# Kernel optimization log

Hardware: AMD Instinct MI355X
Metric: run time of the kernel (lower is better)

Reference implementation:

```python
import jax, jax.numpy as jnp
import numpy as np

RES = 28      # input feature-map resolution
RES2 = 14     # ceil(RES/2) after downsample
NH = 8        # num_heads
KD = 16       # key_dim
D = 64        # attn_ratio * key_dim (per-head value dim)
DH = 512      # D * NH
N = RES * RES
N2 = RES2 * RES2


def _rel_idx():
    # Matches tf.meshgrid default 'xy' indexing in set_attention_bias_idxs.
    r = RES
    kp = np.stack(np.meshgrid(np.arange(r), np.arange(r), indexing='xy')).reshape(2, -1)
    qp = np.stack(np.meshgrid(np.arange(0, r, 2), np.arange(0, r, 2), indexing='xy')).reshape(2, -1)
    rel = np.abs(qp[:, :, None] - kp[:, None, :])
    return jnp.asarray(rel[0] * r + rel[1], dtype=jnp.int32)  # [N2, N]

REL_IDX = _rel_idx()


def _dw_stride2(x, w, b):
    # Depthwise 3x3 conv, stride 2, TF 'SAME' padding. w: [3,3,1,C]
    c = x.shape[-1]
    y = jax.lax.conv_general_dilated(
        x, w, window_strides=(2, 2), padding='SAME',
        dimension_numbers=('NHWC', 'HWIO', 'NHWC'), feature_group_count=c)
    return y + b


def setup_inputs() -> dict:
    key = jax.random.key(0)
    ks = jax.random.split(key, 10)
    f = jnp.float32
    C, OUT = 384, 768
    return {
        'x': jax.random.normal(ks[0], (64, RES, RES, C), f),
        'q_local_w': jax.random.normal(ks[1], (3, 3, 1, C), f) * 0.1,
        'q_local_b': jnp.zeros((C,), f),
        'q_proj_w': jax.random.normal(ks[2], (C, NH * KD), f) * 0.05,
        'q_proj_b': jnp.zeros((NH * KD,), f),
        'q_bn_s': jnp.ones((NH * KD,), f),
        'q_bn_b': jnp.zeros((NH * KD,), f),
        'k_w': jax.random.normal(ks[3], (C, NH * KD), f) * 0.05,
        'k_b': jnp.zeros((NH * KD,), f),
        'k_bn_s': jnp.ones((NH * KD,), f),
        'k_bn_b': jnp.zeros((NH * KD,), f),
        'v_w': jax.random.normal(ks[4], (C, DH), f) * 0.05,
        'v_b': jnp.zeros((DH,), f),
        'v_bn_s': jnp.ones((DH,), f),
        'v_bn_b': jnp.zeros((DH,), f),
        'vloc_w': jax.random.normal(ks[5], (3, 3, 1, DH), f) * 0.1,
        'vloc_b': jnp.zeros((DH,), f),
        'vloc_bn_s': jnp.ones((DH,), f),
        'vloc_bn_b': jnp.zeros((DH,), f),
        'proj_w': jax.random.normal(ks[6], (DH, OUT), f) * 0.05,
        'proj_b': jnp.zeros((OUT,), f),
        'proj_bn_s': jnp.ones((OUT,), f),
        'proj_bn_b': jnp.zeros((OUT,), f),
        'attn_bias': jax.random.normal(ks[7], (NH, N), f) * 0.1,
    }


def reference(x, q_local_w, q_local_b, q_proj_w, q_proj_b, q_bn_s, q_bn_b,
              k_w, k_b, k_bn_s, k_bn_b, v_w, v_b, v_bn_s, v_bn_b,
              vloc_w, vloc_b, vloc_bn_s, vloc_bn_b,
              proj_w, proj_b, proj_bn_s, proj_bn_b, attn_bias):
    B = x.shape[0]
    scale = KD ** -0.5
    # LGQuery: depthwise-conv local branch + 1x1 avg-pool (stride-2 subsample)
    q = _dw_stride2(x, q_local_w, q_local_b) + x[:, ::2, ::2, :]
    q = (q @ q_proj_w + q_proj_b) * q_bn_s + q_bn_b          # [B,14,14,128]
    k = (x @ k_w + k_b) * k_bn_s + k_bn_b                    # [B,28,28,128]
    v = (x @ v_w + v_b) * v_bn_s + v_bn_b                    # [B,28,28,512]
    v_local = _dw_stride2(v, vloc_w, vloc_b) * vloc_bn_s + vloc_bn_b  # [B,14,14,512]
    qh = q.reshape(B, N2, NH, KD).transpose(0, 2, 1, 3)      # [B,H,N2,KD]
    kh = k.reshape(B, N, NH, KD).transpose(0, 2, 3, 1)       # [B,H,KD,N]
    vh = v.reshape(B, N, NH, D).transpose(0, 2, 1, 3)        # [B,H,N,D]
    attn = (qh @ kh) * scale + attn_bias[:, REL_IDX]         # [B,H,N2,N]
    attn = jax.nn.softmax(attn, axis=-1)
    out = (attn @ vh).transpose(0, 2, 1, 3).reshape(B, RES2, RES2, DH)
    out = out + v_local
    # proj: Activation(None) is identity -> 1x1 conv + BN(inference)
    return (out @ proj_w + proj_b) * proj_bn_s + proj_bn_b   # [B,14,14,768]
```

## Files before the change

### kernel.cpp

```cpp
#include <hip/hip_runtime.h>
#include <cstdint>

#define RES    28
#define RES2   14
#define NHEAD  8
#define KDIM   16
#define DV     64
#define DHID   512
#define NSEQ   784
#define N2SEQ  196
#define BATCH  64
#define CIN    384

typedef unsigned short u16;
typedef short  short4_t __attribute__((ext_vector_type(4)));
typedef short  short8_t __attribute__((ext_vector_type(8)));
typedef float  f32x4  __attribute__((ext_vector_type(4)));
typedef u16    us4    __attribute__((ext_vector_type(4)));
typedef u16    us8    __attribute__((ext_vector_type(8)));

__device__ __forceinline__ u16 f2bf(float f) {
    uint32_t u = __float_as_uint(f);
    return (u16)((u + 0x7fffu + ((u >> 16) & 1u)) >> 16);
}
__device__ __forceinline__ float bf2f(u16 h) {
    return __uint_as_float(((uint32_t)h) << 16);
}

__global__ __launch_bounds__(256)
void cast_bf16_kernel(const float* __restrict__ in, u16* __restrict__ out, int n4)
{
    int i = blockIdx.x * 256 + threadIdx.x;
    if (i >= n4) return;
    float4 v = ((const float4*)in)[i];
    us4 r;
    r.x = f2bf(v.x); r.y = f2bf(v.y); r.z = f2bf(v.z); r.w = f2bf(v.w);
    ((us4*)out)[i] = r;
}

__global__ __launch_bounds__(256)
void castT_kernel(const float* __restrict__ W, u16* __restrict__ Wt, int K, int N)
{
    int i = blockIdx.x * 256 + threadIdx.x;
    if (i >= K * N) return;
    int n = i / K, k = i % K;
    Wt[i] = f2bf(W[(size_t)k * N + n]);
}

#define TM 128
#define TN 128
#define TK 32

template<int OUT_BF16>
__global__ __launch_bounds__(256)
void gemm_mfma_kernel(const u16* __restrict__ A, const u16* __restrict__ Bt,
                      const float* __restrict__ bias, const float* __restrict__ scale,
                      const float* __restrict__ shift, void* __restrict__ outp,
                      int M, int N, int K)
{
    __shared__ u16 As[TM * TK];
    __shared__ u16 Bs[TN * TK];

    const int t  = threadIdx.x;
    const int w  = t >> 6;
    const int li = t & 63;
    const int wm = w >> 1, wn = w & 1;
    const int bm = blockIdx.x * TM;
    const int bn = blockIdx.y * TN;
    const int m16 = li & 15;
    const int kg  = li >> 4;

    f32x4 acc[4][4];
    #pragma unroll
    for (int i = 0; i < 4; ++i)
        #pragma unroll
        for (int j = 0; j < 4; ++j) acc[i][j] = (f32x4)0.0f;

    for (int k0 = 0; k0 < K; k0 += TK) {
        #pragma unroll
        for (int i = 0; i < 2; ++i) {
            int c   = (w * 2 + i) * 64 + li;
            int row = c >> 2, kc = c & 3;
            const u16* ag = A  + (size_t)(bm + row) * K + k0 + kc * 8;
            const u16* bg = Bt + (size_t)(bn + row) * K + k0 + kc * 8;
            char* la = (char*)As + (size_t)(w * 2 + i) * 64 * 16;
            char* lb = (char*)Bs + (size_t)(w * 2 + i) * 64 * 16;
            __builtin_amdgcn_global_load_lds(
                (const __attribute__((address_space(1))) void*)ag,
                (__attribute__((address_space(3))) void*)la, 16, 0, 0);
            __builtin_amdgcn_global_load_lds(
                (const __attribute__((address_space(1))) void*)bg,
                (__attribute__((address_space(3))) void*)lb, 16, 0, 0);
        }
        __syncthreads();

        short8_t af[4], bf[4];
        #pragma unroll
        for (int mi = 0; mi < 4; ++mi)
            af[mi] = *(const short8_t*)&As[(wm * 64 + mi * 16 + m16) * TK + kg * 8];
        #pragma unroll
        for (int ni = 0; ni < 4; ++ni)
            bf[ni] = *(const short8_t*)&Bs[(wn * 64 + ni * 16 + m16) * TK + kg * 8];

        #pragma unroll
        for (int mi = 0; mi < 4; ++mi)
            #pragma unroll
            for (int ni = 0; ni < 4; ++ni)
                acc[mi][ni] = __builtin_amdgcn_mfma_f32_16x16x32_bf16(
                    af[mi], bf[ni], acc[mi][ni], 0, 0, 0);
        __syncthreads();
    }

    #pragma unroll
    for (int ni = 0; ni < 4; ++ni) {
        const int col = bn + wn * 64 + ni * 16 + m16;
        const float bi = bias[col], sc = scale[col], sh = shift[col];
        #pragma unroll
        for (int mi = 0; mi < 4; ++mi) {
            const int rbase = bm + wm * 64 + mi * 16 + kg * 4;
            #pragma unroll
            for (int r = 0; r < 4; ++r) {
                float val = (acc[mi][ni][r] + bi) * sc + sh;
                if (OUT_BF16)
                    ((u16*)outp)[(size_t)(rbase + r) * N + col] = f2bf(val);
                else
                    ((float*)outp)[(size_t)(rbase + r) * N + col] = val;
            }
        }
    }
}

__global__ __launch_bounds__(256)
void qin_kernel(const float* __restrict__ x, const float* __restrict__ w,
                const float* __restrict__ b, u16* __restrict__ qin)
{
    const int C4 = CIN / 4;
    int idx = blockIdx.x * 256 + threadIdx.x;
    if (idx >= BATCH * RES2 * RES2 * C4) return;
    int c4 = idx % C4;
    int r  = idx / C4;
    int j  = r % RES2; r /= RES2;
    int i  = r % RES2;
    int bb = r / RES2;

    const float4* x4 = (const float4*)x;
    const float4* w4 = (const float4*)w;
    float4 acc = make_float4(0.f, 0.f, 0.f, 0.f);
    #pragma unroll
    for (int dy = 0; dy < 3; ++dy) {
        int iy = 2 * i + dy;
        if (iy >= RES) continue;
        #pragma unroll
        for (int dx = 0; dx < 3; ++dx) {
            int ix = 2 * j + dx;
            if (ix >= RES) continue;
            float4 xv = x4[((size_t)(bb * RES + iy) * RES + ix) * C4 + c4];
            float4 wv = w4[(dy * 3 + dx) * C4 + c4];
            acc.x += xv.x * wv.x; acc.y += xv.y * wv.y;
            acc.z += xv.z * wv.z; acc.w += xv.w * wv.w;
        }
    }
    float4 bv = ((const float4*)b)[c4];
    float4 xs = x4[((size_t)(bb * RES + 2 * i) * RES + 2 * j) * C4 + c4];
    us4 o;
    o.x = f2bf(acc.x + bv.x + xs.x);
    o.y = f2bf(acc.y + bv.y + xs.y);
    o.z = f2bf(acc.z + bv.z + xs.z);
    o.w = f2bf(acc.w + bv.w + xs.w);
    ((us4*)qin)[idx] = o;
}

__global__ __launch_bounds__(256)
void vloc_kernel(const u16* __restrict__ v, const float* __restrict__ w,
                 const float* __restrict__ b, const float* __restrict__ s,
                 const float* __restrict__ sh, u16* __restrict__ out)
{
    const int C4 = DHID / 4;
    int idx = blockIdx.x * 256 + threadIdx.x;
    if (idx >= BATCH * RES2 * RES2 * C4) return;
    int c4 = idx % C4;
    int r  = idx / C4;
    int j  = r % RES2; r /= RES2;
    int i  = r % RES2;
    int bb = r / RES2;

    const us4* v4 = (const us4*)v;
    const float4* w4 = (const float4*)w;
    float4 acc = make_float4(0.f, 0.f, 0.f, 0.f);
    #pragma unroll
    for (int dy = 0; dy < 3; ++dy) {
        int iy = 2 * i + dy;
        if (iy >= RES) continue;
        #pragma unroll
        for (int dx = 0; dx < 3; ++dx) {
            int ix = 2 * j + dx;
            if (ix >= RES) continue;
            us4 xu = v4[((size_t)(bb * RES + iy) * RES + ix) * C4 + c4];
            float4 wv = w4[(dy * 3 + dx) * C4 + c4];
            acc.x += bf2f(xu.x) * wv.x; acc.y += bf2f(xu.y) * wv.y;
            acc.z += bf2f(xu.z) * wv.z; acc.w += bf2f(xu.w) * wv.w;
        }
    }
    float4 bv = ((const float4*)b)[c4];
    float4 sv = ((const float4*)s)[c4];
    float4 hv = ((const float4*)sh)[c4];
    us4 o;
    o.x = f2bf((acc.x + bv.x) * sv.x + hv.x);
    o.y = f2bf((acc.y + bv.y) * sv.y + hv.y);
    o.z = f2bf((acc.z + bv.z) * sv.z + hv.z);
    o.w = f2bf((acc.w + bv.w) * sv.w + hv.w);
    ((us4*)out)[idx] = o;
}

__global__ __launch_bounds__(256)
void vt_transpose_kernel(const u16* __restrict__ vbuf, u16* __restrict__ vt)
{
    __shared__ u16 tile[64][66];
    const int t  = threadIdx.x;
    const int b  = blockIdx.x;
    const int k0 = blockIdx.y * 64;
    const int h  = blockIdx.z;

    {
        int kr = t >> 2, cc = (t & 3) * 16;
        int key = k0 + kr;
        if (key < NSEQ) {
            const u16* src = vbuf + ((size_t)b * NSEQ + key) * DHID + h * 64 + cc;
            us8 v0 = *(const us8*)src;
            us8 v1 = *(const us8*)(src + 8);
            #pragma unroll
            for (int i = 0; i < 8; ++i) { tile[kr][cc + i] = v0[i]; tile[kr][cc + 8 + i] = v1[i]; }
        }
    }
    __syncthreads();
    {
        int cr = t >> 2, kc = (t & 3) * 16;
        if (k0 + kc < NSEQ) {
            us8 o0, o1;
            #pragma unroll
            for (int i = 0; i < 8; ++i) { o0[i] = tile[kc + i][cr]; o1[i] = tile[kc + 8 + i][cr]; }
            u16* dst = vt + (((size_t)b * NHEAD + h) * 64 + cr) * NSEQ + k0 + kc;
            *(us8*)dst = o0;
            *(us8*)(dst + 8) = o1;
        }
    }
}

__global__ __launch_bounds__(256)
void biasT_kernel(const float* __restrict__ bias, float* __restrict__ biasT)
{
    int tid = blockIdx.x * 256 + threadIdx.x;
    if (tid >= NHEAD * NSEQ * N2SEQ) return;
    int q   = tid % N2SEQ;
    int rem = tid / N2SEQ;
    int key = rem % NSEQ;
    int h   = rem / NSEQ;
    int pi = q / 14, pj = q % 14;
    int ku = key / 28, kw = key % 28;
    int d0 = 2 * pj - kw; if (d0 < 0) d0 = -d0;
    int d1 = 2 * pi - ku; if (d1 < 0) d1 = -d1;
    biasT[tid] = bias[h * NSEQ + d0 * 28 + d1];
}

__global__ __launch_bounds__(128)
void attn_mfma_kernel(const u16* __restrict__ q, const u16* __restrict__ k,
                      const u16* __restrict__ vt, const float* __restrict__ biasT,
                      u16* __restrict__ io)
{
    __shared__ u16 Ks[64 * 16];
    __shared__ u16 Vs[64 * 68];

    const int t    = threadIdx.x;
    const int w    = t >> 6;
    const int lane = t & 63;
    const int col  = lane & 15;
    const int quad = lane >> 4;
    const int bh = blockIdx.x;
    const int b  = bh >> 3;
    const int h  = bh & 7;
    const int qtile = blockIdx.y * 2 + w;
    const bool qvalid = qtile * 16 < N2SEQ;
    const int qbase = qvalid ? qtile * 16 : 192;

    int qq = qbase + col; if (qq > 195) qq = 195;
    short8_t qf = (short8_t)0;
    if (quad < 2)
        qf = *(const short8_t*)(q + ((size_t)(b * N2SEQ + qq) * 128) + h * 16 + quad * 8);

    f32x4 O[4];
    #pragma unroll
    for (int i = 0; i < 4; ++i) O[i] = (f32x4)0.0f;
    float m = -3e38f, l = 0.f;

    const u16* vtb = vt + (size_t)bh * 64 * NSEQ;

    for (int ti = 0; ti < 13; ++ti) {
        const int t0 = ti * 64;
        {
            int c = w * 64 + lane;
            int row = c >> 1;
            int tok = t0 + row; if (tok > 783) tok = 783;
            const u16* src = k + ((size_t)(b * NSEQ + tok) * 128) + h * 16 + (c & 1) * 8;
            char* dst = (char*)Ks + w * 1024;
            __builtin_amdgcn_global_load_lds(
                (const __attribute__((address_space(1))) void*)src,
                (__attribute__((address_space(3))) void*)dst, 16, 0, 0);
        }
        {
            int d = t >> 1, pr = t & 1;
            const u16* src = vtb + (size_t)d * NSEQ;
            u16* dst = Vs + d * 68 + pr * 32;
            #pragma unroll
            for (int i = 0; i < 4; ++i) {
                int kk = t0 + pr * 32 + i * 8; if (kk > 776) kk = 776;
                us8 vv = *(const us8*)(src + kk);
                us4 lo, hi;
                lo.x = vv[0]; lo.y = vv[1]; lo.z = vv[2]; lo.w = vv[3];
                hi.x = vv[4]; hi.y = vv[5]; hi.z = vv[6]; hi.w = vv[7];
                *(us4*)(dst + i * 8)     = lo;
                *(us4*)(dst + i * 8 + 4) = hi;
            }
        }
        __syncthreads();

        f32x4 S[4];
        #pragma unroll
        for (int ks = 0; ks < 4; ++ks) {
            short8_t kf = (short8_t)0;
            if (quad < 2)
                kf = *(const short8_t*)&Ks[(ks * 16 + col) * 16 + quad * 8];
            S[ks] = __builtin_amdgcn_mfma_f32_16x16x32_bf16(kf, qf, (f32x4)0.0f, 0, 0, 0);
        }

        float p[16];
        float mt = -3e38f;
        #pragma unroll
        for (int ks = 0; ks < 4; ++ks) {
            #pragma unroll
            for (int r = 0; r < 4; ++r) {
                int key = t0 + ks * 16 + quad * 4 + r;
                float lg;
                if (key < NSEQ)
                    lg = S[ks][r] * 0.25f + biasT[((size_t)h * NSEQ + key) * N2SEQ + qbase + col];
                else
                    lg = -1e30f;
                p[ks * 4 + r] = lg;
                mt = fmaxf(mt, lg);
            }
        }
        mt = fmaxf(mt, __shfl_xor(mt, 16));
        mt = fmaxf(mt, __shfl_xor(mt, 32));
        float mnew = fmaxf(m, mt);
        float alpha = __expf(m - mnew);
        m = mnew;
        float s = 0.f;
        #pragma unroll
        for (int i = 0; i < 16; ++i) { p[i] = __expf(p[i] - mnew); s += p[i]; }
        s += __shfl_xor(s, 16);
        s += __shfl_xor(s, 32);
        l = l * alpha + s;

        float ar[4];
        #pragma unroll
        for (int r = 0; r < 4; ++r) ar[r] = __shfl(alpha, quad * 4 + r);
        #pragma unroll
        for (int ns = 0; ns < 4; ++ns)
            #pragma unroll
            for (int r = 0; r < 4; ++r) O[ns][r] *= ar[r];

        short8_t pf[2];
        #pragma unroll
        for (int pr = 0; pr < 2; ++pr)
            #pragma unroll
            for (int j = 0; j < 8; ++j)
                pf[pr][j] = (short)f2bf(p[(2 * pr + (j >> 2)) * 4 + (j & 3)]);

        #pragma unroll
        for (int ns = 0; ns < 4; ++ns) {
            #pragma unroll
            for (int pr = 0; pr < 2; ++pr) {
                const u16* vrow = &Vs[(ns * 16 + col) * 68 + pr * 32 + quad * 4];
                us4 v0 = *(const us4*)vrow;
                us4 v1 = *(const us4*)(vrow + 16);
                short8_t vf;
                vf[0] = (short)v0.x; vf[1] = (short)v0.y; vf[2] = (short)v0.z; vf[3] = (short)v0.w;
                vf[4] = (short)v1.x; vf[5] = (short)v1.y; vf[6] = (short)v1.z; vf[7] = (short)v1.w;
                O[ns] = __builtin_amdgcn_mfma_f32_16x16x32_bf16(pf[pr], vf, O[ns], 0, 0, 0);
            }
        }
        __syncthreads();
    }

    float linv = 1.0f / l;
    float lr[4];
    #pragma unroll
    for (int r = 0; r < 4; ++r) lr[r] = __shfl(linv, quad * 4 + r);

    if (qvalid) {
        #pragma unroll
        for (int ns = 0; ns < 4; ++ns) {
            #pragma unroll
            for (int r = 0; r < 4; ++r) {
                int qg2 = qbase + quad * 4 + r;
                if (qg2 < N2SEQ) {
                    size_t a = ((size_t)(b * N2SEQ + qg2) * DHID) + h * 64 + ns * 16 + col;
                    io[a] = f2bf(O[ns][r] * lr[r] + bf2f(io[a]));
                }
            }
        }
    }
}

extern "C" void kernel_launch(void* const* d_in, const int* in_sizes, int n_in,
                              void* d_out, int out_size, void* d_ws, size_t ws_size,
                              hipStream_t stream)
{
    const float* x          = (const float*)d_in[0];
    const float* q_local_w  = (const float*)d_in[1];
    const float* q_local_b  = (const float*)d_in[2];
    const float* q_proj_w   = (const float*)d_in[3];
    const float* q_proj_b   = (const float*)d_in[4];
    const float* q_bn_s     = (const float*)d_in[5];
    const float* q_bn_b     = (const float*)d_in[6];
    const float* k_w        = (const float*)d_in[7];
    const float* k_b        = (const float*)d_in[8];
    const float* k_bn_s     = (const float*)d_in[9];
    const float* k_bn_b     = (const float*)d_in[10];
    const float* v_w        = (const float*)d_in[11];
    const float* v_b        = (const float*)d_in[12];
    const float* v_bn_s     = (const float*)d_in[13];
    const float* v_bn_b     = (const float*)d_in[14];
    const float* vloc_w     = (const float*)d_in[15];
    const float* vloc_b     = (const float*)d_in[16];
    const float* vloc_bn_s  = (const float*)d_in[17];
    const float* vloc_bn_b  = (const float*)d_in[18];
    const float* proj_w     = (const float*)d_in[19];
    const float* proj_b     = (const float*)d_in[20];
    const float* proj_bn_s  = (const float*)d_in[21];
    const float* proj_bn_b  = (const float*)d_in[22];
    const float* attn_bias  = (const float*)d_in[23];
    float* out = (float*)d_out;

    const int M1 = BATCH * NSEQ;
    const int M2 = BATCH * N2SEQ;

    char* p = (char*)d_ws;
    u16* xb     = (u16*)p;
    u16* qin_bf = (u16*)(p + 38535168);
    u16* vt     = (u16*)p;
    size_t off = 51380224;
    u16* kwt = (u16*)(p + off);
    u16* vwt = kwt + (size_t)CIN * 128;
    u16* qwt = vwt + (size_t)CIN * DHID;
    u16* pwt = qwt + (size_t)CIN * 128;
    off += 1376256;
    u16* kbuf = (u16*)(p + off);    off += (size_t)M1 * 128 * 2;
    u16* vbuf = (u16*)(p + off);    off += (size_t)M1 * DHID * 2;
    u16* qbuf = (u16*)(p + off);    off += (size_t)M2 * 128 * 2;
    u16* vloc_bf = (u16*)(p + off); off += (size_t)M2 * DHID * 2;
    float* biasT = (float*)(p + off);

    {
        int n4 = M1 * CIN / 4;
        cast_bf16_kernel<<<dim3((n4 + 255) / 256), 256, 0, stream>>>(x, xb, n4);
    }
    castT_kernel<<<dim3((CIN * 128 + 255) / 256), 256, 0, stream>>>(k_w, kwt, CIN, 128);
    castT_kernel<<<dim3((CIN * DHID + 255) / 256), 256, 0, stream>>>(v_w, vwt, CIN, DHID);
    castT_kernel<<<dim3((CIN * 128 + 255) / 256), 256, 0, stream>>>(q_proj_w, qwt, CIN, 128);
    castT_kernel<<<dim3((DHID * 768 + 255) / 256), 256, 0, stream>>>(proj_w, pwt, DHID, 768);
    biasT_kernel<<<dim3((NHEAD * NSEQ * N2SEQ + 255) / 256), 256, 0, stream>>>(attn_bias, biasT);

    {
        int items = M2 * (CIN / 4);
        qin_kernel<<<dim3((items + 255) / 256), 256, 0, stream>>>(x, q_local_w, q_local_b, qin_bf);
    }
    gemm_mfma_kernel<1><<<dim3(M1 / TM, 128 / TN), 256, 0, stream>>>(
        xb, kwt, k_b, k_bn_s, k_bn_b, kbuf, M1, 128, CIN);
    gemm_mfma_kernel<1><<<dim3(M1 / TM, DHID / TN), 256, 0, stream>>>(
        xb, vwt, v_b, v_bn_s, v_bn_b, vbuf, M1, DHID, CIN);
    gemm_mfma_kernel<1><<<dim3(M2 / TM, 128 / TN), 256, 0, stream>>>(
        qin_bf, qwt, q_proj_b, q_bn_s, q_bn_b, qbuf, M2, 128, CIN);

    vt_transpose_kernel<<<dim3(BATCH, 13, NHEAD), 256, 0, stream>>>(vbuf, vt);

    {
        int items = M2 * (DHID / 4);
        vloc_kernel<<<dim3((items + 255) / 256), 256, 0, stream>>>(
            vbuf, vloc_w, vloc_b, vloc_bn_s, vloc_bn_b, vloc_bf);
    }
    attn_mfma_kernel<<<dim3(BATCH * NHEAD, 7), 128, 0, stream>>>(
        qbuf, kbuf, vt, biasT, vloc_bf);

    gemm_mfma_kernel<0><<<dim3(M2 / TM, 768 / TN), 256, 0, stream>>>(
        vloc_bf, pwt, proj_b, proj_bn_s, proj_bn_b, out, M2, 768, DHID);
}
```

Measured before the change: 450.9 us.

## Restructure attention: one block per batch-head, MFMA-layout bias, head-major Q/K

Each attention block now handles all 13 query tiles of a batch-head with 4 waves, so K/V tiles load into LDS once per batch-head instead of once per pair of query tiles. The relative-position bias is precomputed in MFMA accumulator layout and fed as the MFMA C input, with masking folded in. The 0.25 softmax scale is folded into the Q projection's BN scale and shift. Q and K GEMMs write head-major layout for contiguous loads. In exchange, each thread holds more registers (4 sets of O/m/l), and the grid shrinks to 512 blocks, which may lower occupancy.

```diff
diff --git a/kernel.cpp b/kernel.cpp
--- a/kernel.cpp
+++ b/kernel.cpp
@@ -13,7 +13,6 @@
 #define CIN    384
 
 typedef unsigned short u16;
-typedef short  short4_t __attribute__((ext_vector_type(4)));
 typedef short  short8_t __attribute__((ext_vector_type(8)));
 typedef float  f32x4  __attribute__((ext_vector_type(4)));
 typedef u16    us4    __attribute__((ext_vector_type(4)));
@@ -47,16 +46,57 @@
     Wt[i] = f2bf(W[(size_t)k * N + n]);
 }
 
+__global__ void scale_qsb_kernel(const float* __restrict__ s, const float* __restrict__ b,
+                                 float* __restrict__ o)
+{
+    int i = threadIdx.x;
+    o[i] = 0.25f * s[i];
+    o[128 + i] = 0.25f * b[i];
+}
+
+__global__ __launch_bounds__(256)
+void biasC_kernel(const float* __restrict__ bias, float* __restrict__ biasC)
+{
+    int tid = blockIdx.x * 256 + threadIdx.x;
+    if (tid >= NHEAD * 13 * 4 * 13 * 64) return;
+    int lane = tid & 63;
+    int rem  = tid >> 6;
+    int qt = rem % 13; rem /= 13;
+    int ks = rem % 4;  rem /= 4;
+    int ti = rem % 13;
+    int h  = rem / 13;
+    int col = lane & 15, quad = lane >> 4;
+    int q = qt * 16 + col;
+    float4 out;
+    float* po = &out.x;
+    #pragma unroll
+    for (int r = 0; r < 4; ++r) {
+        int key = ti * 64 + ks * 16 + quad * 4 + r;
+        float v;
+        if (key >= NSEQ || q >= N2SEQ) {
+            v = -1e30f;
+        } else {
+            int pi = q / 14, pj = q % 14;
+            int ku = key / 28, kw = key % 28;
+            int d0 = 2 * pj - kw; if (d0 < 0) d0 = -d0;
+            int d1 = 2 * pi - ku; if (d1 < 0) d1 = -d1;
+            v = bias[h * NSEQ + d0 * 28 + d1];
+        }
+        po[r] = v;
+    }
+    ((float4*)biasC)[tid] = out;
+}
+
 #define TM 128
 #define TN 128
 #define TK 32
 
-template<int OUT_BF16>
+template<int OUT_MODE>
 __global__ __launch_bounds__(256)
 void gemm_mfma_kernel(const u16* __restrict__ A, const u16* __restrict__ Bt,
                       const float* __restrict__ bias, const float* __restrict__ scale,
                       const float* __restrict__ shift, void* __restrict__ outp,
-                      int M, int N, int K)
+                      int M, int N, int K, int rpb)
 {
     __shared__ u16 As[TM * TK];
     __shared__ u16 Bs[TN * TK];
@@ -121,10 +161,16 @@
             #pragma unroll
             for (int r = 0; r < 4; ++r) {
                 float val = (acc[mi][ni][r] + bi) * sc + sh;
-                if (OUT_BF16)
-                    ((u16*)outp)[(size_t)(rbase + r) * N + col] = f2bf(val);
-                else
-                    ((float*)outp)[(size_t)(rbase + r) * N + col] = val;
+                const int row = rbase + r;
+                if (OUT_MODE == 0) {
+                    ((float*)outp)[(size_t)row * N + col] = val;
+                } else if (OUT_MODE == 1) {
+                    ((u16*)outp)[(size_t)row * N + col] = f2bf(val);
+                } else {
+                    int bb = row / rpb, tok = row % rpb;
+                    int hh = col >> 4;
+                    ((u16*)outp)[((size_t)(bb * NHEAD + hh) * rpb + tok) * 16 + (col & 15)] = f2bf(val);
+                }
             }
         }
     }
@@ -246,25 +292,9 @@
     }
 }
 
-__global__ __launch_bounds__(256)
-void biasT_kernel(const float* __restrict__ bias, float* __restrict__ biasT)
-{
-    int tid = blockIdx.x * 256 + threadIdx.x;
-    if (tid >= NHEAD * NSEQ * N2SEQ) return;
-    int q   = tid % N2SEQ;
-    int rem = tid / N2SEQ;
-    int key = rem % NSEQ;
-    int h   = rem / NSEQ;
-    int pi = q / 14, pj = q % 14;
-    int ku = key / 28, kw = key % 28;
-    int d0 = 2 * pj - kw; if (d0 < 0) d0 = -d0;
-    int d1 = 2 * pi - ku; if (d1 < 0) d1 = -d1;
-    biasT[tid] = bias[h * NSEQ + d0 * 28 + d1];
-}
-
-__global__ __launch_bounds__(128)
+__global__ __launch_bounds__(256, 2)
 void attn_mfma_kernel(const u16* __restrict__ q, const u16* __restrict__ k,
-                      const u16* __restrict__ vt, const float* __restrict__ biasT,
+                      const u16* __restrict__ vt, const float* __restrict__ biasC,
                       u16* __restrict__ io)
 {
     __shared__ u16 Ks[64 * 16];
@@ -275,138 +305,163 @@
     const int lane = t & 63;
     const int col  = lane & 15;
     const int quad = lane >> 4;
-    const int bh = blockIdx.x;
-    const int b  = bh >> 3;
-    const int h  = bh & 7;
-    const int qtile = blockIdx.y * 2 + w;
-    const bool qvalid = qtile * 16 < N2SEQ;
-    const int qbase = qvalid ? qtile * 16 : 192;
-
-    int qq = qbase + col; if (qq > 195) qq = 195;
-    short8_t qf = (short8_t)0;
-    if (quad < 2)
-        qf = *(const short8_t*)(q + ((size_t)(b * N2SEQ + qq) * 128) + h * 16 + quad * 8);
-
-    f32x4 O[4];
-    #pragma unroll
-    for (int i = 0; i < 4; ++i) O[i] = (f32x4)0.0f;
-    float m = -3e38f, l = 0.f;
+    const int h  = blockIdx.x >> 6;
+    const int b  = blockIdx.x & 63;
+    const int bh = b * NHEAD + h;
+
+    short8_t qf[4];
+    #pragma unroll
+    for (int i = 0; i < 4; ++i) {
+        int qt = w + 4 * i;
+        qf[i] = (short8_t)0;
+        if (qt < 13 && quad < 2) {
+            int qq = qt * 16 + col; if (qq > 195) qq = 195;
+            qf[i] = *(const short8_t*)(q + ((size_t)bh * N2SEQ + qq) * 16 + quad * 8);
+        }
+    }
+
+    f32x4 O[4][4];
+    float m[4], l[4];
+    #pragma unroll
+    for (int i = 0; i < 4; ++i) {
+        m[i] = -3e38f; l[i] = 0.f;
+        #pragma unroll
+        for (int ns = 0; ns < 4; ++ns) O[i][ns] = (f32x4)0.0f;
+    }
 
     const u16* vtb = vt + (size_t)bh * 64 * NSEQ;
+    const u16* kb  = k + (size_t)bh * NSEQ * 16;
 
     for (int ti = 0; ti < 13; ++ti) {
         const int t0 = ti * 64;
-        {
+        if (w < 2) {
             int c = w * 64 + lane;
-            int row = c >> 1;
-            int tok = t0 + row; if (tok > 783) tok = 783;
-            const u16* src = k + ((size_t)(b * NSEQ + tok) * 128) + h * 16 + (c & 1) * 8;
+            int tok = t0 + (c >> 1); if (tok > 783) tok = 783;
+            const u16* src = kb + (size_t)tok * 16 + (c & 1) * 8;
             char* dst = (char*)Ks + w * 1024;
             __builtin_amdgcn_global_load_lds(
                 (const __attribute__((address_space(1))) void*)src,
                 (__attribute__((address_space(3))) void*)dst, 16, 0, 0);
         }
         {
-            int d = t >> 1, pr = t & 1;
+            int d = t >> 2, part = t & 3;
             const u16* src = vtb + (size_t)d * NSEQ;
-            u16* dst = Vs + d * 68 + pr * 32;
-            #pragma unroll
-            for (int i = 0; i < 4; ++i) {
-                int kk = t0 + pr * 32 + i * 8; if (kk > 776) kk = 776;
-                us8 vv = *(const us8*)(src + kk);
-                us4 lo, hi;
-                lo.x = vv[0]; lo.y = vv[1]; lo.z = vv[2]; lo.w = vv[3];
-                hi.x = vv[4]; hi.y = vv[5]; hi.z = vv[6]; hi.w = vv[7];
-                *(us4*)(dst + i * 8)     = lo;
-                *(us4*)(dst + i * 8 + 4) = hi;
-            }
+            u16* dst = Vs + d * 68 + part * 16;
+            int kk = t0 + part * 16;
+            int k0a = kk     > 776 ? 776 : kk;
+            int k1a = kk + 8 > 776 ? 776 : kk + 8;
+            us8 v0 = *(const us8*)(src + k0a);
+            us8 v1 = *(const us8*)(src + k1a);
+            us4 a, bb2, c2, d2;
+            a.x = v0[0]; a.y = v0[1]; a.z = v0[2]; a.w = v0[3];
+            bb2.x = v0[4]; bb2.y = v0[5]; bb2.z = v0[6]; bb2.w = v0[7];
+            c2.x = v1[0]; c2.y = v1[1]; c2.z = v1[2]; c2.w = v1[3];
+            d2.x = v1[4]; d2.y = v1[5]; d2.z = v1[6]; d2.w = v1[7];
+            *(us4*)(dst)      = a;
+            *(us4*)(dst + 4)  = bb2;
+            *(us4*)(dst + 8)  = c2;
+            *(us4*)(dst + 12) = d2;
         }
         __syncthreads();
 
-        f32x4 S[4];
+        short8_t kf[4];
         #pragma unroll
         for (int ks = 0; ks < 4; ++ks) {
-            short8_t kf = (short8_t)0;
+            kf[ks] = (short8_t)0;
             if (quad < 2)
-                kf = *(const short8_t*)&Ks[(ks * 16 + col) * 16 + quad * 8];
-            S[ks] = __builtin_amdgcn_mfma_f32_16x16x32_bf16(kf, qf, (f32x4)0.0f, 0, 0, 0);
-        }
-
-        float p[16];
-        float mt = -3e38f;
-        #pragma unroll
-        for (int ks = 0; ks < 4; ++ks) {
-            #pragma unroll
-            for (int r = 0; r < 4; ++r) {
-                int key = t0 + ks * 16 + quad * 4 + r;
-                float lg;
-                if (key < NSEQ)
-                    lg = S[ks][r] * 0.25f + biasT[((size_t)h * NSEQ + key) * N2SEQ + qbase + col];
-                else
-                    lg = -1e30f;
-                p[ks * 4 + r] = lg;
-                mt = fmaxf(mt, lg);
-            }
-        }
-        mt = fmaxf(mt, __shfl_xor(mt, 16));
-        mt = fmaxf(mt, __shfl_xor(mt, 32));
-        float mnew = fmaxf(m, mt);
-        float alpha = __expf(m - mnew);
-        m = mnew;
-        float s = 0.f;
-        #pragma unroll
-        for (int i = 0; i < 16; ++i) { p[i] = __expf(p[i] - mnew); s += p[i]; }
-        s += __shfl_xor(s, 16);
-        s += __shfl_xor(s, 32);
-        l = l * alpha + s;
-
-        float ar[4];
-        #pragma unroll
-        for (int r = 0; r < 4; ++r) ar[r] = __shfl(alpha, quad * 4 + r);
+                kf[ks] = *(const short8_t*)&Ks[(ks * 16 + col) * 16 + quad * 8];
+        }
+        short8_t vf[4][2];
         #pragma unroll
         for (int ns = 0; ns < 4; ++ns)
-            #pragma unroll
-            for (int r = 0; r < 4; ++r) O[ns][r] *= ar[r];
-
-        short8_t pf[2];
-        #pragma unroll
-        for (int pr = 0; pr < 2; ++pr)
-            #pragma unroll
-            for (int j = 0; j < 8; ++j)
-                pf[pr][j] = (short)f2bf(p[(2 * pr + (j >> 2)) * 4 + (j & 3)]);
-
-        #pragma unroll
-        for (int ns = 0; ns < 4; ++ns) {
             #pragma unroll
             for (int pr = 0; pr < 2; ++pr) {
                 const u16* vrow = &Vs[(ns * 16 + col) * 68 + pr * 32 + quad * 4];
                 us4 v0 = *(const us4*)vrow;
                 us4 v1 = *(const us4*)(vrow + 16);
-                short8_t vf;
-                vf[0] = (short)v0.x; vf[1] = (short)v0.y; vf[2] = (short)v0.z; vf[3] = (short)v0.w;
-                vf[4] = (short)v1.x; vf[5] = (short)v1.y; vf[6] = (short)v1.z; vf[7] = (short)v1.w;
-                O[ns] = __builtin_amdgcn_mfma_f32_16x16x32_bf16(pf[pr], vf, O[ns], 0, 0, 0);
+                short8_t vv;
+                vv[0] = (short)v0.x; vv[1] = (short)v0.y; vv[2] = (short)v0.z; vv[3] = (short)v0.w;
+                vv[4] = (short)v1.x; vv[5] = (short)v1.y; vv[6] = (short)v1.z; vv[7] = (short)v1.w;
+                vf[ns][pr] = vv;
             }
+
+        #pragma unroll
+        for (int i = 0; i < 4; ++i) {
+            int qt = w + 4 * i;
+            if (qt < 13) {
+                f32x4 S[4];
+                #pragma unroll
+                for (int ks = 0; ks < 4; ++ks) {
+                    f32x4 c = *(const f32x4*)(biasC +
+                        ((((size_t)h * 13 + ti) * 4 + ks) * 13 + qt) * 256 + lane * 4);
+                    S[ks] = __builtin_amdgcn_mfma_f32_16x16x32_bf16(kf[ks], qf[i], c, 0, 0, 0);
+                }
+                float p[16];
+                float mt = -3e38f;
+                #pragma unroll
+                for (int ks = 0; ks < 4; ++ks)
+                    #pragma unroll
+                    for (int r = 0; r < 4; ++r) {
+                        float lg = S[ks][r];
+                        p[ks * 4 + r] = lg;
+                        mt = fmaxf(mt, lg);
+                    }
+                mt = fmaxf(mt, __shfl_xor(mt, 16));
+                mt = fmaxf(mt, __shfl_xor(mt, 32));
+                float mnew = fmaxf(m[i], mt);
+                float alpha = __expf(m[i] - mnew);
+                m[i] = mnew;
+                float s = 0.f;
+                #pragma unroll
+                for (int j = 0; j < 16; ++j) { p[j] = __expf(p[j] - mnew); s += p[j]; }
+                s += __shfl_xor(s, 16);
+                s += __shfl_xor(s, 32);
+                l[i] = l[i] * alpha + s;
+
+                float ar[4];
+                #pragma unroll
+                for (int r = 0; r < 4; ++r) ar[r] = __shfl(alpha, quad * 4 + r);
+                #pragma unroll
+                for (int ns = 0; ns < 4; ++ns)
+                    #pragma unroll
+                    for (int r = 0; r < 4; ++r) O[i][ns][r] *= ar[r];
+
+                short8_t pf[2];
+                #pragma unroll
+                for (int pr = 0; pr < 2; ++pr)
+                    #pragma unroll
+                    for (int j = 0; j < 8; ++j)
+                        pf[pr][j] = (short)f2bf(p[(2 * pr + (j >> 2)) * 4 + (j & 3)]);
+
+                #pragma unroll
+                for (int ns = 0; ns < 4; ++ns)
+                    #pragma unroll
+                    for (int pr = 0; pr < 2; ++pr)
+                        O[i][ns] = __builtin_amdgcn_mfma_f32_16x16x32_bf16(
+                            pf[pr], vf[ns][pr], O[i][ns], 0, 0, 0);
+            }
         }
         __syncthreads();
     }
 
-    float linv = 1.0f / l;
-    float lr[4];
-    #pragma unroll
-    for (int r = 0; r < 4; ++r) lr[r] = __shfl(linv, quad * 4 + r);
-
-    if (qvalid) {
-        #pragma unroll
-        for (int ns = 0; ns < 4; ++ns) {
-            #pragma unroll
-            for (int r = 0; r < 4; ++r) {
-                int qg2 = qbase + quad * 4 + r;
-                if (qg2 < N2SEQ) {
-                    size_t a = ((size_t)(b * N2SEQ + qg2) * DHID) + h * 64 + ns * 16 + col;
-                    io[a] = f2bf(O[ns][r] * lr[r] + bf2f(io[a]));
+    #pragma unroll
+    for (int i = 0; i < 4; ++i) {
+        int qt = w + 4 * i;
+        if (qt < 13) {
+            float linv = 1.0f / l[i];
+            float lr[4];
+            #pragma unroll
+            for (int r = 0; r < 4; ++r) lr[r] = __shfl(linv, quad * 4 + r);
+            #pragma unroll
+            for (int ns = 0; ns < 4; ++ns)
+                #pragma unroll
+                for (int r = 0; r < 4; ++r) {
+                    int q2 = qt * 16 + quad * 4 + r;
+                    if (q2 < N2SEQ) {
+                        size_t a = ((size_t)(b * N2SEQ + q2) * DHID) + h * 64 + ns * 16 + col;
+                        io[a] = f2bf(O[i][ns][r] * lr[r] + bf2f(io[a]));
+                    }
                 }
-            }
         }
     }
 }
@@ -458,7 +513,8 @@
     u16* vbuf = (u16*)(p + off);    off += (size_t)M1 * DHID * 2;
     u16* qbuf = (u16*)(p + off);    off += (size_t)M2 * 128 * 2;
     u16* vloc_bf = (u16*)(p + off); off += (size_t)M2 * DHID * 2;
-    float* biasT = (float*)(p + off);
+    float* biasC = (float*)(p + off); off += (size_t)NHEAD * 13 * 4 * 13 * 256 * 4;
+    float* qsb  = (float*)(p + off);
 
     {
         int n4 = M1 * CIN / 4;
@@ -468,18 +524,21 @@
     castT_kernel<<<dim3((CIN * DHID + 255) / 256), 256, 0, stream>>>(v_w, vwt, CIN, DHID);
     castT_kernel<<<dim3((CIN * 128 + 255) / 256), 256, 0, stream>>>(q_proj_w, qwt, CIN, 128);
     castT_kernel<<<dim3((DHID * 768 + 255) / 256), 256, 0, stream>>>(proj_w, pwt, DHID, 768);
-    biasT_kernel<<<dim3((NHEAD * NSEQ * N2SEQ + 255) / 256), 256, 0, stream>>>(attn_bias, biasT);
-
+    scale_qsb_kernel<<<dim3(1), 128, 0, stream>>>(q_bn_s, q_bn_b, qsb);
+    {
+        int items = NHEAD * 13 * 4 * 13 * 64;
+        biasC_kernel<<<dim3((items + 255) / 256), 256, 0, stream>>>(attn_bias, biasC);
+    }
     {
         int items = M2 * (CIN / 4);
         qin_kernel<<<dim3((items + 255) / 256), 256, 0, stream>>>(x, q_local_w, q_local_b, qin_bf);
     }
-    gemm_mfma_kernel<1><<<dim3(M1 / TM, 128 / TN), 256, 0, stream>>>(
-        xb, kwt, k_b, k_bn_s, k_bn_b, kbuf, M1, 128, CIN);
+    gemm_mfma_kernel<2><<<dim3(M1 / TM, 128 / TN), 256, 0, stream>>>(
+        xb, kwt, k_b, k_bn_s, k_bn_b, kbuf, M1, 128, CIN, NSEQ);
     gemm_mfma_kernel<1><<<dim3(M1 / TM, DHID / TN), 256, 0, stream>>>(
-        xb, vwt, v_b, v_bn_s, v_bn_b, vbuf, M1, DHID, CIN);
-    gemm_mfma_kernel<1><<<dim3(M2 / TM, 128 / TN), 256, 0, stream>>>(
-        qin_bf, qwt, q_proj_b, q_bn_s, q_bn_b, qbuf, M2, 128, CIN);
+        xb, vwt, v_b, v_bn_s, v_bn_b, vbuf, M1, DHID, CIN, 0);
+    gemm_mfma_kernel<2><<<dim3(M2 / TM, 128 / TN), 256, 0, stream>>>(
+        qin_bf, qwt, q_proj_b, qsb, qsb + 128, qbuf, M2, 128, CIN, N2SEQ);
 
     vt_transpose_kernel<<<dim3(BATCH, 13, NHEAD), 256, 0, stream>>>(vbuf, vt);
 
@@ -488,9 +547,9 @@
         vloc_kernel<<<dim3((items + 255) / 256), 256, 0, stream>>>(
             vbuf, vloc_w, vloc_b, vloc_bn_s, vloc_bn_b, vloc_bf);
     }
-    attn_mfma_kernel<<<dim3(BATCH * NHEAD, 7), 128, 0, stream>>>(
-        qbuf, kbuf, vt, biasT, vloc_bf);
+    attn_mfma_kernel<<<dim3(NHEAD * BATCH), 256, 0, stream>>>(
+        qbuf, kbuf, vt, biasC, vloc_bf);
 
     gemm_mfma_kernel<0><<<dim3(M2 / TM, 768 / TN), 256, 0, stream>>>(
-        vloc_bf, pwt, proj_b, proj_bn_s, proj_bn_b, out, M2, 768, DHID);
-}
+        vloc_bf, pwt, proj_b, proj_bn_s, proj_bn_b, out, M2, 768, DHID, 0);
+}
```

Measured after the change: 423.1 us. 1.07x faster.
